# Performance work log

Hardware: AMD Instinct MI355X
Metric: run time of the kernel (lower is better)

The kernel has to match this reference:

```python
import jax, jax.numpy as jnp
import numpy as np
from jax import lax

DIM = 8        # per-head dim
HEADS = 32     # inp // dim
EPS = 1e-15    # linear-attention eps
BN_EPS = 1e-5  # torch BatchNorm2d default eps


def _conv(x, w, groups=1, pad=0):
    return lax.conv_general_dilated(
        x, w, window_strides=(1, 1), padding=[(pad, pad), (pad, pad)],
        feature_group_count=groups,
        dimension_numbers=('NCHW', 'OIHW', 'NCHW'))


def setup_inputs() -> dict:
    key = jax.random.key(0)
    ks = jax.random.split(key, 9)
    B, C, H, W = 8, 256, 64, 64
    td = HEADS * DIM  # 256
    x = jax.random.normal(ks[0], (B, C, H, W), jnp.float32)
    w_qkv = jax.random.normal(ks[1], (3 * td, C, 1, 1), jnp.float32) * 0.05
    w_dw = jax.random.normal(ks[2], (3 * td, 1, 5, 5), jnp.float32) * 0.05
    w_pw = jax.random.normal(ks[3], (3 * td, (3 * td) // (3 * HEADS), 1, 1), jnp.float32) * 0.05
    w_proj = jax.random.normal(ks[4], (C, 2 * td, 1, 1), jnp.float32) * 0.05
    bn_gamma = 1.0 + 0.1 * jax.random.normal(ks[5], (C,), jnp.float32)
    bn_beta = 0.1 * jax.random.normal(ks[6], (C,), jnp.float32)
    bn_mean = 0.1 * jax.random.normal(ks[7], (C,), jnp.float32)
    bn_var = jnp.ones((C,), jnp.float32)
    return dict(x=x, w_qkv=w_qkv, w_dw=w_dw, w_pw=w_pw, w_proj=w_proj,
                bn_gamma=bn_gamma, bn_beta=bn_beta, bn_mean=bn_mean, bn_var=bn_var)


def reference(x, w_qkv, w_dw, w_pw, w_proj, bn_gamma, bn_beta, bn_mean, bn_var):
    B, _, H, W = x.shape
    # qkv: 1x1 conv, no bias/norm/act
    qkv = _conv(x, w_qkv)                                   # (B, 3*td, H, W)
    # aggreg branch: depthwise 5x5 then grouped 1x1 (groups = 3*heads)
    agg = _conv(qkv, w_dw, groups=w_dw.shape[0], pad=2)
    agg = _conv(agg, w_pw, groups=3 * HEADS)
    ms = jnp.concatenate([qkv, agg], axis=1)                # (B, 2*3*td, H, W)
    # relu linear attention
    G = ms.shape[1] // (3 * DIM)                            # 2*heads = 64
    t = ms.reshape(B, G, 3 * DIM, H * W).transpose(0, 1, 3, 2)  # (B, G, N, 3d)
    q = jax.nn.relu(t[..., :DIM])
    k = jax.nn.relu(t[..., DIM:2 * DIM])
    v = t[..., 2 * DIM:]
    v = jnp.pad(v, ((0, 0), (0, 0), (0, 0), (0, 1)), constant_values=1.0)  # ones trick
    kv = jnp.einsum('bgnd,bgne->bgde', k, v)                # (B, G, d, d+1)
    out = jnp.einsum('bgnd,bgde->bgne', q, kv)              # (B, G, N, d+1)
    out = out[..., :-1] / (out[..., -1:] + EPS)
    out = out.transpose(0, 1, 3, 2).reshape(B, G * DIM, H, W)  # (B, 2*td, H, W)
    # proj: 1x1 conv + BatchNorm2d (eval mode), no act
    out = _conv(out, w_proj)
    inv = jax.lax.rsqrt(bn_var + BN_EPS)
    out = (out - bn_mean[:, None, None]) * (inv * bn_gamma)[:, None, None] + bn_beta[:, None, None]
    return out
```

## Files before the change

### kernel.cpp

```cpp
#include <hip/hip_runtime.h>

typedef __bf16 bf16;
typedef __bf16 bf16x4 __attribute__((ext_vector_type(4)));
typedef __bf16 bf16x8 __attribute__((ext_vector_type(8)));
typedef float f32x4 __attribute__((ext_vector_type(4)));

#define NPIX 4096

__global__ __launch_bounds__(256) void split_x(
    const float* __restrict__ x,
    bf16* __restrict__ xTh, bf16* __restrict__ xTm, bf16* __restrict__ xTl)
{
    const int pix = blockIdx.x * 256 + threadIdx.x;
    const int k0  = blockIdx.y * 32;
    const int b   = blockIdx.z;

    const float* __restrict__ src = x + ((size_t)b * 256 + k0) * NPIX + pix;
    float v[32];
#pragma unroll
    for (int kk = 0; kk < 32; ++kk) v[kk] = src[(size_t)kk * NPIX];

    const size_t drow = ((size_t)b * NPIX + pix) * 256 + k0;
#pragma unroll
    for (int c = 0; c < 4; ++c) {
        bf16x8 vh, vm, vl;
#pragma unroll
        for (int j = 0; j < 8; ++j) {
            float val = v[c * 8 + j];
            bf16 h = (bf16)val; float r  = val - (float)h;
            bf16 m = (bf16)r;   float r2 = r - (float)m;
            vh[j] = h; vm[j] = m; vl[j] = (bf16)r2;
        }
        *(bf16x8*)(xTh + drow + c * 8) = vh;
        *(bf16x8*)(xTm + drow + c * 8) = vm;
        *(bf16x8*)(xTl + drow + c * 8) = vl;
    }
}

__global__ __launch_bounds__(256) void split_w3(
    const float* __restrict__ w,
    bf16* __restrict__ h, bf16* __restrict__ m, bf16* __restrict__ l)
{
    const int i = blockIdx.x * 256 + threadIdx.x;
    const float v = w[i];
    const bf16 a = (bf16)v;  const float r1 = v - (float)a;
    const bf16 c = (bf16)r1;
    h[i] = a; m[i] = c; l[i] = (bf16)(r1 - (float)c);
}

__global__ __launch_bounds__(256) void split_w2(
    const float* __restrict__ w, bf16* __restrict__ h, bf16* __restrict__ m)
{
    const int i = blockIdx.x * 256 + threadIdx.x;
    const float v = w[i];
    const bf16 a = (bf16)v;
    h[i] = a; m[i] = (bf16)(v - (float)a);
}

__global__ __launch_bounds__(256, 2) void qkv_mfma(
    const bf16* __restrict__ Ah, const bf16* __restrict__ Am,
    const bf16* __restrict__ Al,
    const bf16* __restrict__ xTh, const bf16* __restrict__ xTm,
    const bf16* __restrict__ xTl,
    float* __restrict__ C)
{
    __shared__ __align__(16) bf16 As[2][3][128][32];

    const int tid  = threadIdx.x;
    const int lane = tid & 63;
    const int wv   = tid >> 6;
    const int col  = lane & 15;
    const int quad = lane >> 4;
    const int wm   = (wv >> 1) * 64;
    const int wn   = (wv & 1) * 64;
    const int n0   = blockIdx.x * 128;
    const int m0   = blockIdx.y * 128;
    const int b    = blockIdx.z;

    const size_t xoff = ((size_t)b * NPIX + n0 + wn) * 256;

    const int srow = wv * 16 + (lane >> 2);
    const int schk = (lane & 3) * 8;

    const bf16* AP[3] = {Ah, Am, Al};

    auto stage = [&](int buf, int kk) {
#pragma unroll
        for (int p = 0; p < 3; ++p)
#pragma unroll
            for (int hh = 0; hh < 2; ++hh) {
                const bf16* gp = AP[p] + (size_t)(m0 + hh * 64 + srow) * 256 + kk + schk;
                __builtin_amdgcn_global_load_lds(
                    (const __attribute__((address_space(1))) void*)gp,
                    (__attribute__((address_space(3))) void*)&As[buf][p][hh * 64 + wv * 16][0],
                    16, 0, 0);
            }
    };

    f32x4 acc[4][4] = {};

    stage(0, 0);
    bf16x8 bh[4], bl[4], bm[4];
#pragma unroll
    for (int t = 0; t < 4; ++t) {
        const size_t brow = xoff + (size_t)(t * 16 + col) * 256 + 0 + quad * 8;
        bh[t] = *(const bf16x8*)(xTh + brow);
        bl[t] = *(const bf16x8*)(xTl + brow);
        bm[t] = *(const bf16x8*)(xTm + brow);
    }

#pragma unroll
    for (int k0 = 0; k0 < 256; k0 += 32) {
        const int cur = (k0 >> 5) & 1;
        const bool more = (k0 + 32 < 256);

        __syncthreads();

        bf16x8 af[4][3];
#pragma unroll
        for (int s = 0; s < 4; ++s)
#pragma unroll
            for (int p = 0; p < 3; ++p)
                af[s][p] = *(const bf16x8*)&As[cur][p][wm + s * 16 + col][quad * 8];

        bf16x8 nbh[4], nbl[4], nbm[4];
        if (more) {
            stage(cur ^ 1, k0 + 32);
#pragma unroll
            for (int t = 0; t < 4; ++t) {
                const size_t brow = xoff + (size_t)(t * 16 + col) * 256 + (k0 + 32) + quad * 8;
                nbh[t] = *(const bf16x8*)(xTh + brow);
                nbl[t] = *(const bf16x8*)(xTl + brow);
                nbm[t] = *(const bf16x8*)(xTm + brow);
            }
        }

#pragma unroll
        for (int t = 0; t < 4; ++t)
#pragma unroll
            for (int s = 0; s < 4; ++s)
                acc[s][t] = __builtin_amdgcn_mfma_f32_16x16x32_bf16(af[s][2], bh[t], acc[s][t], 0, 0, 0);
#pragma unroll
        for (int t = 0; t < 4; ++t)
#pragma unroll
            for (int s = 0; s < 4; ++s)
                acc[s][t] = __builtin_amdgcn_mfma_f32_16x16x32_bf16(af[s][0], bl[t], acc[s][t], 0, 0, 0);
#pragma unroll
        for (int t = 0; t < 4; ++t)
#pragma unroll
            for (int s = 0; s < 4; ++s)
                acc[s][t] = __builtin_amdgcn_mfma_f32_16x16x32_bf16(af[s][1], bm[t], acc[s][t], 0, 0, 0);
#pragma unroll
        for (int t = 0; t < 4; ++t)
#pragma unroll
            for (int s = 0; s < 4; ++s)
                acc[s][t] = __builtin_amdgcn_mfma_f32_16x16x32_bf16(af[s][1], bh[t], acc[s][t], 0, 0, 0);
#pragma unroll
        for (int t = 0; t < 4; ++t)
#pragma unroll
            for (int s = 0; s < 4; ++s)
                acc[s][t] = __builtin_amdgcn_mfma_f32_16x16x32_bf16(af[s][0], bm[t], acc[s][t], 0, 0, 0);
#pragma unroll
        for (int t = 0; t < 4; ++t)
#pragma unroll
            for (int s = 0; s < 4; ++s)
                acc[s][t] = __builtin_amdgcn_mfma_f32_16x16x32_bf16(af[s][0], bh[t], acc[s][t], 0, 0, 0);

        if (more) {
#pragma unroll
            for (int t = 0; t < 4; ++t) {
                bh[t] = nbh[t]; bl[t] = nbl[t]; bm[t] = nbm[t];
            }
        }
    }

    float* __restrict__ Cp = C + (size_t)b * 768 * NPIX;
#pragma unroll
    for (int s = 0; s < 4; ++s)
#pragma unroll
        for (int t = 0; t < 4; ++t)
#pragma unroll
            for (int r = 0; r < 4; ++r) {
                const int m = m0 + wm + s * 16 + quad * 4 + r;
                const int n = n0 + wn + t * 16 + col;
                Cp[(size_t)m * NPIX + n] = acc[s][t][r];
            }
}

__global__ __launch_bounds__(256) void dwpw(
    const float* __restrict__ qkv,
    const float* __restrict__ w_dw,
    const float* __restrict__ w_pw,
    float* __restrict__ agg)
{
    __shared__ float sm[8][20][72];

    const int tid = threadIdx.x;
    const int y0  = blockIdx.x * 16;
    const int p   = blockIdx.y;
    const int b   = blockIdx.z;

    const float* __restrict__ src = qkv + ((size_t)b * 768 + 8 * p) * NPIX;

#pragma unroll
    for (int it = 0; it < 10; ++it) {
        int idx = tid + it * 256;
        int c  = idx / 320;
        int r  = idx % 320;
        int sy = r >> 4;
        int x4 = (r & 15) * 4;
        int gy = y0 + sy - 2;
        float4 v = {0.f, 0.f, 0.f, 0.f};
        if ((unsigned)gy < 64u)
            v = *(const float4*)(src + (size_t)c * NPIX + gy * 64 + x4);
        *(float4*)&sm[c][sy][4 + x4] = v;
    }
    if (tid < 160) {
        int c = tid / 20, sy = tid % 20;
        sm[c][sy][2] = 0.f; sm[c][sy][3] = 0.f;
        sm[c][sy][68] = 0.f; sm[c][sy][69] = 0.f;
    }
    __syncthreads();

    const int ty = tid >> 4;
    const int x0 = (tid & 15) * 4;

    float d[8][4];
#pragma unroll
    for (int c = 0; c < 8; ++c) {
        float a0 = 0.f, a1 = 0.f, a2 = 0.f, a3 = 0.f;
        const float* __restrict__ wc = w_dw + (size_t)(8 * p + c) * 25;
#pragma unroll
        for (int ky = 0; ky < 5; ++ky) {
            float r[12];
            *(float4*)&r[0] = *(const float4*)&sm[c][ty + ky][x0];
            *(float4*)&r[4] = *(const float4*)&sm[c][ty + ky][x0 + 4];
            *(float4*)&r[8] = *(const float4*)&sm[c][ty + ky][x0 + 8];
#pragma unroll
            for (int kx = 0; kx < 5; ++kx) {
                const float wv = wc[ky * 5 + kx];
                a0 = fmaf(wv, r[2 + 0 + kx], a0);
                a1 = fmaf(wv, r[2 + 1 + kx], a1);
                a2 = fmaf(wv, r[2 + 2 + kx], a2);
                a3 = fmaf(wv, r[2 + 3 + kx], a3);
            }
        }
        d[c][0] = a0; d[c][1] = a1; d[c][2] = a2; d[c][3] = a3;
    }

    float* __restrict__ dst = agg + ((size_t)b * 768 + 8 * p) * NPIX + (y0 + ty) * 64 + x0;
#pragma unroll
    for (int o = 0; o < 8; ++o) {
        const float* __restrict__ wo = w_pw + (size_t)(8 * p + o) * 8;
        float4 s = {0.f, 0.f, 0.f, 0.f};
#pragma unroll
        for (int i = 0; i < 8; ++i) {
            const float wv = wo[i];
            s.x = fmaf(wv, d[i][0], s.x);
            s.y = fmaf(wv, d[i][1], s.y);
            s.z = fmaf(wv, d[i][2], s.z);
            s.w = fmaf(wv, d[i][3], s.w);
        }
        *(float4*)(dst + (size_t)o * NPIX) = s;
    }
}

__global__ __launch_bounds__(256) void kv_reduce(
    const float* __restrict__ qkv, const float* __restrict__ agg,
    float* __restrict__ kvb)
{
    const int g = blockIdx.x, b = blockIdx.y;
    const float* __restrict__ src = (g < 32) ? qkv : agg;
    const float* __restrict__ base = src + ((size_t)b * 768 + 24 * (g & 31)) * NPIX;

    float acc[72];
#pragma unroll
    for (int i = 0; i < 72; ++i) acc[i] = 0.0f;

    for (int i4 = threadIdx.x; i4 < NPIX / 4; i4 += 256) {
        float4 kf[8], vf[8];
#pragma unroll
        for (int d = 0; d < 8; ++d) {
            float4 t = ((const float4*)(base + (size_t)(8 + d) * NPIX))[i4];
            kf[d].x = fmaxf(0.0f, t.x); kf[d].y = fmaxf(0.0f, t.y);
            kf[d].z = fmaxf(0.0f, t.z); kf[d].w = fmaxf(0.0f, t.w);
        }
#pragma unroll
        for (int e = 0; e < 8; ++e)
            vf[e] = ((const float4*)(base + (size_t)(16 + e) * NPIX))[i4];
#pragma unroll
        for (int d = 0; d < 8; ++d) {
#pragma unroll
            for (int e = 0; e < 8; ++e)
                acc[d * 9 + e] += kf[d].x * vf[e].x + kf[d].y * vf[e].y +
                                  kf[d].z * vf[e].z + kf[d].w * vf[e].w;
            acc[d * 9 + 8] += kf[d].x + kf[d].y + kf[d].z + kf[d].w;
        }
    }

    const int lane = threadIdx.x & 63;
    const int wv   = threadIdx.x >> 6;
#pragma unroll
    for (int i = 0; i < 72; ++i) {
        float v = acc[i];
        v += __shfl_xor(v, 32, 64);
        v += __shfl_xor(v, 16, 64);
        v += __shfl_xor(v, 8, 64);
        v += __shfl_xor(v, 4, 64);
        v += __shfl_xor(v, 2, 64);
        v += __shfl_xor(v, 1, 64);
        acc[i] = v;
    }
    __shared__ float red[4][72];
    if (lane == 0) {
#pragma unroll
        for (int i = 0; i < 72; ++i) red[wv][i] = acc[i];
    }
    __syncthreads();
    if (threadIdx.x < 72)
        kvb[((size_t)b * 64 + g) * 72 + threadIdx.x] =
            red[0][threadIdx.x] + red[1][threadIdx.x] +
            red[2][threadIdx.x] + red[3][threadIdx.x];
}

__global__ __launch_bounds__(256) void attn_fused(
    const float* __restrict__ qkv, const float* __restrict__ agg,
    const float* __restrict__ kvb,
    bf16* __restrict__ attTh, bf16* __restrict__ attTm)
{
    const int b   = blockIdx.y;
    const int n0  = blockIdx.x * 32;
    const int tid = threadIdx.x;
    const int p   = tid & 31;
    const int c   = tid >> 5;

    __shared__ float kvs[64 * 72];
    for (int i = tid; i < 64 * 72; i += 256) kvs[i] = kvb[(size_t)b * 64 * 72 + i];
    __syncthreads();

    const int n = n0 + p;
    const size_t orow = ((size_t)b * NPIX + n) * 512;

#pragma unroll
    for (int gi = 0; gi < 8; ++gi) {
        const int g = c * 8 + gi;
        const float* __restrict__ src = (g < 32) ? qkv : agg;
        const float* __restrict__ base = src + ((size_t)b * 768 + 24 * (g & 31)) * NPIX + n;

        float q[8];
#pragma unroll
        for (int d = 0; d < 8; ++d) q[d] = fmaxf(0.0f, base[(size_t)d * NPIX]);

        const float* kv = &kvs[g * 72];
        float den = 1e-15f;
#pragma unroll
        for (int d = 0; d < 8; ++d) den = fmaf(q[d], kv[d * 9 + 8], den);
        float inv = 1.0f / den;
#pragma unroll
        for (int d = 0; d < 8; ++d) q[d] *= inv;

        bf16x8 vh, vm;
#pragma unroll
        for (int e = 0; e < 8; ++e) {
            float o = 0.0f;
#pragma unroll
            for (int d = 0; d < 8; ++d) o = fmaf(q[d], kv[d * 9 + e], o);
            bf16 h = (bf16)o;
            vh[e] = h;
            vm[e] = (bf16)(o - (float)h);
        }
        *(bf16x8*)(attTh + orow + g * 8) = vh;
        *(bf16x8*)(attTm + orow + g * 8) = vm;
    }
}

__global__ __launch_bounds__(256, 2) void proj_mfma(
    const bf16* __restrict__ Ph, const bf16* __restrict__ Pm,
    const bf16* __restrict__ Bh, const bf16* __restrict__ Bm,
    float* __restrict__ C,
    const float* __restrict__ bn_g, const float* __restrict__ bn_b,
    const float* __restrict__ bn_m, const float* __restrict__ bn_v)
{
    __shared__ __align__(16) bf16 As[2][2][128][32];

    const int tid  = threadIdx.x;
    const int lane = tid & 63;
    const int wv   = tid >> 6;
    const int col  = lane & 15;
    const int quad = lane >> 4;
    const int wm   = (wv >> 1) * 64;
    const int wn   = (wv & 1) * 64;
    const int n0   = blockIdx.x * 128;
    const int m0   = blockIdx.y * 128;
    const int b    = blockIdx.z;

    const size_t boff = ((size_t)b * NPIX + n0 + wn) * 512;

    const int srow = wv * 16 + (lane >> 2);
    const int schk = (lane & 3) * 8;

    const bf16* AP[2] = {Ph, Pm};

    auto stage = [&](int buf, int kk) {
#pragma unroll
        for (int p = 0; p < 2; ++p)
#pragma unroll
            for (int hh = 0; hh < 2; ++hh) {
                const bf16* gp = AP[p] + (size_t)(m0 + hh * 64 + srow) * 512 + kk + schk;
                __builtin_amdgcn_global_load_lds(
                    (const __attribute__((address_space(1))) void*)gp,
                    (__attribute__((address_space(3))) void*)&As[buf][p][hh * 64 + wv * 16][0],
                    16, 0, 0);
            }
    };

    f32x4 acc[4][4] = {};

    stage(0, 0);
    bf16x8 bh[4], bm2[4];
#pragma unroll
    for (int t = 0; t < 4; ++t) {
        const size_t brow = boff + (size_t)(t * 16 + col) * 512 + 0 + quad * 8;
        bh[t]  = *(const bf16x8*)(Bh + brow);
        bm2[t] = *(const bf16x8*)(Bm + brow);
    }

#pragma unroll
    for (int k0 = 0; k0 < 512; k0 += 32) {
        const int cur = (k0 >> 5) & 1;
        const bool more = (k0 + 32 < 512);

        __syncthreads();

        bf16x8 af0[4], af1[4];
#pragma unroll
        for (int s = 0; s < 4; ++s) {
            af0[s] = *(const bf16x8*)&As[cur][0][wm + s * 16 + col][quad * 8];
            af1[s] = *(const bf16x8*)&As[cur][1][wm + s * 16 + col][quad * 8];
        }

        bf16x8 nbh[4], nbm[4];
        if (more) {
            stage(cur ^ 1, k0 + 32);
#pragma unroll
            for (int t = 0; t < 4; ++t) {
                const size_t brow = boff + (size_t)(t * 16 + col) * 512 + (k0 + 32) + quad * 8;
                nbh[t] = *(const bf16x8*)(Bh + brow);
                nbm[t] = *(const bf16x8*)(Bm + brow);
            }
        }

#pragma unroll
        for (int t = 0; t < 4; ++t)
#pragma unroll
            for (int s = 0; s < 4; ++s)
                acc[s][t] = __builtin_amdgcn_mfma_f32_16x16x32_bf16(af1[s], bh[t], acc[s][t], 0, 0, 0);
#pragma unroll
        for (int t = 0; t < 4; ++t)
#pragma unroll
            for (int s = 0; s < 4; ++s)
                acc[s][t] = __builtin_amdgcn_mfma_f32_16x16x32_bf16(af0[s], bm2[t], acc[s][t], 0, 0, 0);
#pragma unroll
        for (int t = 0; t < 4; ++t)
#pragma unroll
            for (int s = 0; s < 4; ++s)
                acc[s][t] = __builtin_amdgcn_mfma_f32_16x16x32_bf16(af0[s], bh[t], acc[s][t], 0, 0, 0);

        if (more) {
#pragma unroll
            for (int t = 0; t < 4; ++t) {
                bh[t] = nbh[t]; bm2[t] = nbm[t];
            }
        }
    }

    float* __restrict__ Cp = C + (size_t)b * 256 * NPIX;
#pragma unroll
    for (int s = 0; s < 4; ++s) {
#pragma unroll
        for (int r = 0; r < 4; ++r) {
            const int m = m0 + wm + s * 16 + quad * 4 + r;
            const float sc  = (1.0f / sqrtf(bn_v[m] + 1e-5f)) * bn_g[m];
            const float off = bn_b[m] - bn_m[m] * sc;
#pragma unroll
            for (int t = 0; t < 4; ++t) {
                const int n = n0 + wn + t * 16 + col;
                Cp[(size_t)m * NPIX + n] = acc[s][t][r] * sc + off;
            }
        }
    }
}

extern "C" void kernel_launch(void* const* d_in, const int* in_sizes, int n_in,
                              void* d_out, int out_size, void* d_ws, size_t ws_size,
                              hipStream_t stream) {
    const float* x      = (const float*)d_in[0];
    const float* w_qkv  = (const float*)d_in[1];
    const float* w_dw   = (const float*)d_in[2];
    const float* w_pw   = (const float*)d_in[3];
    const float* w_proj = (const float*)d_in[4];
    const float* bn_g   = (const float*)d_in[5];
    const float* bn_b   = (const float*)d_in[6];
    const float* bn_m   = (const float*)d_in[7];
    const float* bn_v   = (const float*)d_in[8];
    float* out = (float*)d_out;

    char* ws = (char*)d_ws;
    float* qkv  = (float*)ws;
    float* agg  = (float*)(ws + 100663296ull);
    char*  r3   = ws + 201326592ull;
    bf16*  xTh  = (bf16*)r3;
    bf16*  xTm  = (bf16*)(r3 + 16777216ull);
    bf16*  xTl  = (bf16*)(r3 + 33554432ull);
    bf16*  wqh  = (bf16*)(r3 + 50331648ull);
    bf16*  wqm  = (bf16*)(r3 + 50331648ull + 393216ull);
    bf16*  wql  = (bf16*)(r3 + 50331648ull + 786432ull);
    bf16*  attTh = (bf16*)r3;
    bf16*  attTm = (bf16*)(r3 + 33554432ull);
    bf16*  wph  = (bf16*)ws;
    bf16*  wpm  = (bf16*)(ws + 262144ull);
    float* kvb  = (float*)d_out;

    split_x<<<dim3(16, 8, 8), dim3(256), 0, stream>>>(x, xTh, xTm, xTl);

    split_w3<<<dim3(768), dim3(256), 0, stream>>>(w_qkv, wqh, wqm, wql);

    qkv_mfma<<<dim3(32, 6, 8), dim3(256), 0, stream>>>(
        wqh, wqm, wql, xTh, xTm, xTl, qkv);

    dwpw<<<dim3(4, 96, 8), dim3(256), 0, stream>>>(qkv, w_dw, w_pw, agg);

    kv_reduce<<<dim3(64, 8), dim3(256), 0, stream>>>(qkv, agg, kvb);

    attn_fused<<<dim3(128, 8), dim3(256), 0, stream>>>(qkv, agg, kvb, attTh, attTm);

    split_w2<<<dim3(512), dim3(256), 0, stream>>>(w_proj, wph, wpm);

    proj_mfma<<<dim3(32, 2, 8), dim3(256), 0, stream>>>(
        wph, wpm, attTh, attTm, out, bn_g, bn_b, bn_m, bn_v);
}
```

Before: 414.3 us.

## Split kv reduction across pixel chunks and vectorize attention over four pixels

kv_reduce now launches four chunks per group and batch, each thread handling one float4 of pixels, and writes partial kv sums that attn_fused adds together when it loads them into shared memory. attn_fused is regridded so each block covers 16 groups and 128 pixels, with each thread doing four adjacent pixels through float4 loads. The goal is more parallelism in the reduction, which previously ran on only 512 blocks each looping over all pixels, and wider loads in the attention pass. In exchange, every attention block re-reads and sums four partial kv buffers, and the bf16 stores become per-pixel writes with a 1KB stride.

```diff
diff --git a/kernel.cpp b/kernel.cpp
--- a/kernel.cpp
+++ b/kernel.cpp
@@ -267,35 +267,33 @@
 
 __global__ __launch_bounds__(256) void kv_reduce(
     const float* __restrict__ qkv, const float* __restrict__ agg,
-    float* __restrict__ kvb)
-{
-    const int g = blockIdx.x, b = blockIdx.y;
+    float* __restrict__ kvp)
+{
+    const int g = blockIdx.x, chunk = blockIdx.y, b = blockIdx.z;
     const float* __restrict__ src = (g < 32) ? qkv : agg;
     const float* __restrict__ base = src + ((size_t)b * 768 + 24 * (g & 31)) * NPIX;
 
+    const int i4 = chunk * 256 + threadIdx.x;
+
+    float4 kf[8], vf[8];
+#pragma unroll
+    for (int d = 0; d < 8; ++d) {
+        float4 t = ((const float4*)(base + (size_t)(8 + d) * NPIX))[i4];
+        kf[d].x = fmaxf(0.0f, t.x); kf[d].y = fmaxf(0.0f, t.y);
+        kf[d].z = fmaxf(0.0f, t.z); kf[d].w = fmaxf(0.0f, t.w);
+    }
+#pragma unroll
+    for (int e = 0; e < 8; ++e)
+        vf[e] = ((const float4*)(base + (size_t)(16 + e) * NPIX))[i4];
+
     float acc[72];
 #pragma unroll
-    for (int i = 0; i < 72; ++i) acc[i] = 0.0f;
-
-    for (int i4 = threadIdx.x; i4 < NPIX / 4; i4 += 256) {
-        float4 kf[8], vf[8];
-#pragma unroll
-        for (int d = 0; d < 8; ++d) {
-            float4 t = ((const float4*)(base + (size_t)(8 + d) * NPIX))[i4];
-            kf[d].x = fmaxf(0.0f, t.x); kf[d].y = fmaxf(0.0f, t.y);
-            kf[d].z = fmaxf(0.0f, t.z); kf[d].w = fmaxf(0.0f, t.w);
-        }
+    for (int d = 0; d < 8; ++d) {
 #pragma unroll
         for (int e = 0; e < 8; ++e)
-            vf[e] = ((const float4*)(base + (size_t)(16 + e) * NPIX))[i4];
-#pragma unroll
-        for (int d = 0; d < 8; ++d) {
-#pragma unroll
-            for (int e = 0; e < 8; ++e)
-                acc[d * 9 + e] += kf[d].x * vf[e].x + kf[d].y * vf[e].y +
-                                  kf[d].z * vf[e].z + kf[d].w * vf[e].w;
-            acc[d * 9 + 8] += kf[d].x + kf[d].y + kf[d].z + kf[d].w;
-        }
+            acc[d * 9 + e] = kf[d].x * vf[e].x + kf[d].y * vf[e].y +
+                             kf[d].z * vf[e].z + kf[d].w * vf[e].w;
+        acc[d * 9 + 8] = kf[d].x + kf[d].y + kf[d].z + kf[d].w;
     }
 
     const int lane = threadIdx.x & 63;
@@ -318,59 +316,91 @@
     }
     __syncthreads();
     if (threadIdx.x < 72)
-        kvb[((size_t)b * 64 + g) * 72 + threadIdx.x] =
+        kvp[(((size_t)chunk * 8) + b) * 4608 + (size_t)g * 72 + threadIdx.x] =
             red[0][threadIdx.x] + red[1][threadIdx.x] +
             red[2][threadIdx.x] + red[3][threadIdx.x];
 }
 
 __global__ __launch_bounds__(256) void attn_fused(
     const float* __restrict__ qkv, const float* __restrict__ agg,
-    const float* __restrict__ kvb,
+    const float* __restrict__ kvp,
     bf16* __restrict__ attTh, bf16* __restrict__ attTm)
 {
-    const int b   = blockIdx.y;
-    const int n0  = blockIdx.x * 32;
+    const int b   = blockIdx.z;
+    const int gq  = blockIdx.y * 16;
+    const int n0  = blockIdx.x * 128;
     const int tid = threadIdx.x;
     const int p   = tid & 31;
-    const int c   = tid >> 5;
-
-    __shared__ float kvs[64 * 72];
-    for (int i = tid; i < 64 * 72; i += 256) kvs[i] = kvb[(size_t)b * 64 * 72 + i];
+    const int c2  = tid >> 5;
+
+    __shared__ float kvs[16 * 72];
+    for (int i = tid; i < 16 * 72; i += 256) {
+        const size_t gidx = (size_t)gq * 72 + i;
+        kvs[i] = kvp[(0ull * 8 + b) * 4608 + gidx] +
+                 kvp[(1ull * 8 + b) * 4608 + gidx] +
+                 kvp[(2ull * 8 + b) * 4608 + gidx] +
+                 kvp[(3ull * 8 + b) * 4608 + gidx];
+    }
     __syncthreads();
 
-    const int n = n0 + p;
-    const size_t orow = ((size_t)b * NPIX + n) * 512;
-
-#pragma unroll
-    for (int gi = 0; gi < 8; ++gi) {
-        const int g = c * 8 + gi;
+    const int n = n0 + p * 4;
+
+#pragma unroll
+    for (int gi = 0; gi < 2; ++gi) {
+        const int g = gq + c2 * 2 + gi;
         const float* __restrict__ src = (g < 32) ? qkv : agg;
         const float* __restrict__ base = src + ((size_t)b * 768 + 24 * (g & 31)) * NPIX + n;
 
-        float q[8];
-#pragma unroll
-        for (int d = 0; d < 8; ++d) q[d] = fmaxf(0.0f, base[(size_t)d * NPIX]);
-
-        const float* kv = &kvs[g * 72];
-        float den = 1e-15f;
-#pragma unroll
-        for (int d = 0; d < 8; ++d) den = fmaf(q[d], kv[d * 9 + 8], den);
-        float inv = 1.0f / den;
-#pragma unroll
-        for (int d = 0; d < 8; ++d) q[d] *= inv;
-
-        bf16x8 vh, vm;
+        f32x4 q[8];
+#pragma unroll
+        for (int d = 0; d < 8; ++d) {
+            f32x4 t = *(const f32x4*)(base + (size_t)d * NPIX);
+#pragma unroll
+            for (int j = 0; j < 4; ++j) q[d][j] = fmaxf(0.0f, t[j]);
+        }
+
+        const float* kv = &kvs[(c2 * 2 + gi) * 72];
+        f32x4 den = {1e-15f, 1e-15f, 1e-15f, 1e-15f};
+#pragma unroll
+        for (int d = 0; d < 8; ++d) {
+            const float kd = kv[d * 9 + 8];
+#pragma unroll
+            for (int j = 0; j < 4; ++j) den[j] = fmaf(q[d][j], kd, den[j]);
+        }
+        f32x4 inv;
+#pragma unroll
+        for (int j = 0; j < 4; ++j) inv[j] = 1.0f / den[j];
+#pragma unroll
+        for (int d = 0; d < 8; ++d)
+#pragma unroll
+            for (int j = 0; j < 4; ++j) q[d][j] *= inv[j];
+
+        f32x4 o[8];
 #pragma unroll
         for (int e = 0; e < 8; ++e) {
-            float o = 0.0f;
-#pragma unroll
-            for (int d = 0; d < 8; ++d) o = fmaf(q[d], kv[d * 9 + e], o);
-            bf16 h = (bf16)o;
-            vh[e] = h;
-            vm[e] = (bf16)(o - (float)h);
-        }
-        *(bf16x8*)(attTh + orow + g * 8) = vh;
-        *(bf16x8*)(attTm + orow + g * 8) = vm;
+            o[e] = f32x4{0.f, 0.f, 0.f, 0.f};
+#pragma unroll
+            for (int d = 0; d < 8; ++d) {
+                const float kd = kv[d * 9 + e];
+#pragma unroll
+                for (int j = 0; j < 4; ++j) o[e][j] = fmaf(q[d][j], kd, o[e][j]);
+            }
+        }
+
+#pragma unroll
+        for (int j = 0; j < 4; ++j) {
+            bf16x8 vh, vm;
+#pragma unroll
+            for (int e = 0; e < 8; ++e) {
+                const float val = o[e][j];
+                bf16 h = (bf16)val;
+                vh[e] = h;
+                vm[e] = (bf16)(val - (float)h);
+            }
+            const size_t orow = ((size_t)b * NPIX + n + j) * 512;
+            *(bf16x8*)(attTh + orow + g * 8) = vh;
+            *(bf16x8*)(attTm + orow + g * 8) = vm;
+        }
     }
 }
 
@@ -519,7 +549,7 @@
     bf16*  attTm = (bf16*)(r3 + 33554432ull);
     bf16*  wph  = (bf16*)ws;
     bf16*  wpm  = (bf16*)(ws + 262144ull);
-    float* kvb  = (float*)d_out;
+    float* kvp  = (float*)d_out;
 
     split_x<<<dim3(16, 8, 8), dim3(256), 0, stream>>>(x, xTh, xTm, xTl);
 
@@ -530,9 +560,10 @@
 
     dwpw<<<dim3(4, 96, 8), dim3(256), 0, stream>>>(qkv, w_dw, w_pw, agg);
 
-    kv_reduce<<<dim3(64, 8), dim3(256), 0, stream>>>(qkv, agg, kvb);
-
-    attn_fused<<<dim3(128, 8), dim3(256), 0, stream>>>(qkv, agg, kvb, attTh, attTm);
+    kv_reduce<<<dim3(64, 4, 8), dim3(256), 0, stream>>>(qkv, agg, kvp);
+
+    attn_fused<<<dim3(32, 4, 8), dim3(256), 0, stream>>>(
+        qkv, agg, kvp, attTh, attTm);
 
     split_w2<<<dim3(512), dim3(256), 0, stream>>>(w_proj, wph, wpm);
 
```

New measurement: 414.6 us. About the same (+0.1%).
